# Performance work log

Hardware: AMD Instinct MI355X
Metric: run time of the kernel (lower is better)

Reference implementation:

```python
import jax, jax.numpy as jnp
import numpy as np

NUM_HEADS = 8
WINDOW = 3
LOCAL_LEN = WINDOW * WINDOW
SR_RATIO = 8


def _normalize(v, eps=1e-12):
    n = jnp.linalg.norm(v, axis=-1, keepdims=True)
    return v / jnp.maximum(n, eps)


def _layernorm(v, g, b, eps=1e-5):
    m = v.mean(-1, keepdims=True)
    var = ((v - m) ** 2).mean(-1, keepdims=True)
    return (v - m) / jnp.sqrt(var + eps) * g + b


def _unfold3(x, H, W):
    # x: [B, C, H, W] -> [B, C, 9, H*W]  (kernel 3, pad 1, stride 1; torch nn.Unfold layout)
    B, C = x.shape[0], x.shape[1]
    xp = jnp.pad(x, ((0, 0), (0, 0), (1, 1), (1, 1)))
    patches = jnp.stack([xp[:, :, di:di + H, dj:dj + W]
                         for di in range(WINDOW) for dj in range(WINDOW)], axis=2)
    return patches.reshape(B, C, LOCAL_LEN, H * W)


def _forward(x, relative_coords_table, seq_length_scale, q_w, q_b, kv_w, kv_b,
             temperature, query_embedding, sr_w, sr_b, norm_g, norm_b,
             cpb_fc1_w, cpb_fc1_b, cpb_fc2_w, cpb_fc2_b,
             rel_bias_local, learnable_tokens, learnable_bias,
             proj_w, proj_b, relative_pos_index, padding_mask, H, W):
    B, N, C = x.shape
    hd = C // NUM_HEADS
    pool_H, pool_W = H // SR_RATIO, W // SR_RATIO
    pool_len = pool_H * pool_W

    # ---- queries ----
    q = (x @ q_w.T + q_b).reshape(B, N, NUM_HEADS, hd).transpose(0, 2, 1, 3)  # [B,h,N,d]
    q_norm = _normalize(q)
    q_scaled = (q_norm + query_embedding) * jax.nn.softplus(temperature) * seq_length_scale

    # ---- local k/v via unfold ----
    kv = x @ kv_w.T + kv_b  # [B,N,2C]
    k_loc = _normalize(kv[..., :C].reshape(B, N, NUM_HEADS, hd)).reshape(B, N, C)
    kv_img = jnp.concatenate([k_loc, kv[..., C:]], -1).transpose(0, 2, 1).reshape(B, 2 * C, H, W)
    kv_unf = _unfold3(kv_img, H, W).reshape(B, 2 * NUM_HEADS, hd, LOCAL_LEN, N)
    kv_unf = kv_unf.transpose(0, 1, 4, 2, 3)  # [B,2h,N,d,9]
    k_local, v_local = kv_unf[:, :NUM_HEADS], kv_unf[:, NUM_HEADS:]

    attn_local = jnp.einsum('bhnd,bhndl->bhnl', q_scaled, k_local) + rel_bias_local[:, None, :]
    attn_local = jnp.where(padding_mask, -jnp.inf, attn_local)

    # ---- pooled global k/v ----
    x_img = x.transpose(0, 2, 1).reshape(B, C, H, W)
    x_sr = jax.nn.gelu(jnp.einsum('oc,bchw->bohw', sr_w, x_img) + sr_b[None, :, None, None],
                       approximate=False)
    x_pool = x_sr.reshape(B, C, pool_H, SR_RATIO, pool_W, SR_RATIO).mean((3, 5))
    x_pool = x_pool.reshape(B, C, pool_len).transpose(0, 2, 1)
    x_pool = _layernorm(x_pool, norm_g, norm_b)
    kv_p = (x_pool @ kv_w.T + kv_b).reshape(B, pool_len, 2 * NUM_HEADS, hd).transpose(0, 2, 1, 3)
    k_pool, v_pool = kv_p[:, :NUM_HEADS], kv_p[:, NUM_HEADS:]

    # ---- continuous relative position bias (extrapolation path) ----
    cpb = jax.nn.relu(relative_coords_table @ cpb_fc1_w.T + cpb_fc1_b) @ cpb_fc2_w.T + cpb_fc2_b  # [T,h]
    pool_bias = cpb[relative_pos_index].reshape(N, pool_len, NUM_HEADS).transpose(2, 0, 1)  # [h,N,P]

    attn_pool = jnp.einsum('bhnd,bhpd->bhnp', q_scaled, _normalize(k_pool)) + pool_bias

    attn = jax.nn.softmax(jnp.concatenate([attn_local, attn_pool], -1), axis=-1)
    a_loc, a_pool = attn[..., :LOCAL_LEN], attn[..., LOCAL_LEN:]

    lt = jnp.einsum('bhnd,hdl->bhnl', q_norm, learnable_tokens) + learnable_bias + a_loc
    x_local = jnp.einsum('bhnl,bhndl->bhnd', lt, v_local)
    x_p = jnp.einsum('bhnp,bhpd->bhnd', a_pool, v_pool)
    out = (x_local + x_p).transpose(0, 2, 1, 3).reshape(B, N, C)
    return out @ proj_w.T + proj_b


def setup_inputs() -> dict:
    key = jax.random.key(0)
    B, H, W, C = 4, 64, 64, 256
    N = H * W
    hd = C // NUM_HEADS
    pool_H, pool_W = H // SR_RATIO, W // SR_RATIO
    pool_len = pool_H * pool_W

    # padding mask + per-query valid window length (get_seqlen_and_mask)
    ii, jj = np.meshgrid(np.arange(H), np.arange(W), indexing='ij')
    cols = []
    for di in range(WINDOW):
        for dj in range(WINDOW):
            ni, nj = ii + di - 1, jj + dj - 1
            cols.append(((ni < 0) | (ni >= H) | (nj < 0) | (nj >= W)).reshape(-1))
    padding_mask = np.stack(cols, -1)  # [N, 9], True = outside image
    local_len = (~padding_mask).sum(-1, keepdims=True).astype(np.float32)
    seq_length_scale = np.log(local_len + pool_len)  # [N, 1]

    # get_relative_position_cpb((H,W), (pool_H,pool_W))
    axis_q = np.arange(H, dtype=np.float64)
    axis_k = axis_q.reshape(pool_H, SR_RATIO).mean(-1)
    kh, kw = np.meshgrid(axis_k, axis_k, indexing='ij')
    qh, qw = np.meshgrid(axis_q, axis_q, indexing='ij')
    rel_h = (qh.ravel()[:, None] - kh.ravel()[None, :]) / (H - 1) * 8
    rel_w = (qw.ravel()[:, None] - kw.ravel()[None, :]) / (W - 1) * 8
    rel = np.stack([rel_h, rel_w], -1).reshape(-1, 2)
    table, idx = np.unique(rel, axis=0, return_inverse=True)
    table = np.sign(table) * np.log2(np.abs(table) + 1.0) / np.log2(8.0)

    ks = jax.random.split(key, 12)

    def nrm(k, shape, std=0.02):
        return jax.random.normal(k, shape, jnp.float32) * std

    return {
        'x': jax.random.normal(ks[0], (B, N, C), jnp.float32),
        'relative_coords_table': jnp.asarray(table, jnp.float32),
        'seq_length_scale': jnp.asarray(seq_length_scale, jnp.float32),
        'q_w': nrm(ks[1], (C, C)), 'q_b': jnp.zeros((C,), jnp.float32),
        'kv_w': nrm(ks[2], (2 * C, C)), 'kv_b': jnp.zeros((2 * C,), jnp.float32),
        'temperature': jnp.full((NUM_HEADS, 1, 1), float(np.log(np.expm1(1.0 / 0.24))), jnp.float32),
        'query_embedding': nrm(ks[3], (NUM_HEADS, 1, hd)),
        'sr_w': nrm(ks[4], (C, C)), 'sr_b': jnp.zeros((C,), jnp.float32),
        'norm_g': jnp.ones((C,), jnp.float32), 'norm_b': jnp.zeros((C,), jnp.float32),
        'cpb_fc1_w': nrm(ks[5], (512, 2), 0.1), 'cpb_fc1_b': jnp.zeros((512,), jnp.float32),
        'cpb_fc2_w': nrm(ks[6], (NUM_HEADS, 512)), 'cpb_fc2_b': jnp.zeros((NUM_HEADS,), jnp.float32),
        'rel_bias_local': nrm(ks[7], (NUM_HEADS, LOCAL_LEN), 0.0004),
        'learnable_tokens': nrm(ks[8], (NUM_HEADS, hd, LOCAL_LEN)),
        'learnable_bias': jnp.zeros((NUM_HEADS, 1, LOCAL_LEN), jnp.float32),
        'proj_w': nrm(ks[9], (C, C)), 'proj_b': jnp.zeros((C,), jnp.float32),
        'relative_pos_index': jnp.asarray(idx, jnp.int32),
        'padding_mask': jnp.asarray(padding_mask),
        'H': H, 'W': W,
    }


def reference(x, relative_coords_table, seq_length_scale, q_w, q_b, kv_w, kv_b,
              temperature, query_embedding, sr_w, sr_b, norm_g, norm_b,
              cpb_fc1_w, cpb_fc1_b, cpb_fc2_w, cpb_fc2_b,
              rel_bias_local, learnable_tokens, learnable_bias,
              proj_w, proj_b, relative_pos_index, padding_mask, H, W):
    return _forward(x, relative_coords_table, seq_length_scale, q_w, q_b, kv_w, kv_b,
                    temperature, query_embedding, sr_w, sr_b, norm_g, norm_b,
                    cpb_fc1_w, cpb_fc1_b, cpb_fc2_w, cpb_fc2_b,
                    rel_bias_local, learnable_tokens, learnable_bias,
                    proj_w, proj_b, relative_pos_index, padding_mask, H, W)
```

## Files before the change

### kernel.cpp

```cpp
#include <hip/hip_runtime.h>
#include <math.h>


typedef unsigned short ushort_t;
typedef __attribute__((ext_vector_type(8))) _Float16 half8;
typedef __attribute__((ext_vector_type(2))) _Float16 half2_t;
typedef __attribute__((ext_vector_type(4))) float f32x4;
typedef __attribute__((ext_vector_type(4))) int int4_t;

static __device__ __forceinline__ ushort_t f2h(float f) {
    _Float16 h = (_Float16)f;
    return *(ushort_t*)&h;
}

static __device__ __forceinline__ float fdot2f(half2_t a, half2_t b, float c) {
#if __has_builtin(__builtin_amdgcn_fdot2)
    return __builtin_amdgcn_fdot2(a, b, c, false);
#else
    return (float)a[0] * (float)b[0] + (float)a[1] * (float)b[1] + c;
#endif
}

template <int CTRL>
static __device__ __forceinline__ float dpp_addf(float x) {
    int v = __builtin_amdgcn_update_dpp(
        0, __builtin_bit_cast(int, x), CTRL, 0xF, 0xF, true);
    return x + __builtin_bit_cast(float, v);
}
template <int CTRL>
static __device__ __forceinline__ float dpp_maxf(float x) {
    int v = __builtin_amdgcn_update_dpp(
        0, __builtin_bit_cast(int, x), CTRL, 0xF, 0xF, true);
    return fmaxf(x, __builtin_bit_cast(float, v));
}
static __device__ __forceinline__ float quad_sumf(float x) {
    return dpp_addf<0x4E>(dpp_addf<0xB1>(x));
}
static __device__ __forceinline__ float sum16f(float x) {
    return dpp_addf<0x128>(dpp_addf<0x124>(quad_sumf(x)));
}
static __device__ __forceinline__ float max16f(float x) {
    return dpp_maxf<0x128>(dpp_maxf<0x124>(dpp_maxf<0x4E>(dpp_maxf<0xB1>(x))));
}

#define GLOAD16(g, l)                                                        \
    __builtin_amdgcn_global_load_lds(                                        \
        (const __attribute__((address_space(1))) unsigned int*)(g),          \
        (__attribute__((address_space(3))) unsigned int*)(l), 16, 0, 0)

template <int TM, int TN, bool AHM>
__global__ __launch_bounds__(256) void mfma_hgemm(
    const ushort_t* __restrict__ Ag, const ushort_t* __restrict__ Bg,
    const float* __restrict__ bias, float* __restrict__ out0,
    ushort_t* __restrict__ qh_out, ushort_t* __restrict__ kvh,
    ushort_t* __restrict__ xsrh, int mode, int Arows)
{
    const int K = 256;
    const int IM = TM / 32;
    const int JN = TN / 32;
    constexpr int LPS = TM / 64 + TN / 64;
    __shared__ ushort_t Ah[2][TM * 32];
    __shared__ ushort_t Bh[2][TN * 32];

    const int t = threadIdx.x;
    const int w = t >> 6;
    const int lane = t & 63;

    const int nwg = gridDim.x * gridDim.y;
    int wg = blockIdx.y * gridDim.x + blockIdx.x;
    wg = (wg & 7) * (nwg >> 3) + (wg >> 3);
    const int bm = (wg / gridDim.x) * TM;
    const int bn = (wg % gridDim.x) * TN;

    const int wm = (w >> 1) * (TM / 2);
    const int wn = (w & 1) * (TN / 2);

    f32x4 acc[IM][JN];
#pragma unroll
    for (int i = 0; i < IM; ++i)
#pragma unroll
        for (int j = 0; j < JN; ++j) acc[i][j] = f32x4{0.f, 0.f, 0.f, 0.f};

    const int lrow  = t >> 2;
    const int lk8sw = ((t & 3) ^ ((t >> 3) & 3)) * 8;

#define STAGE(bufi, k0s)                                                     \
    do {                                                                     \
        _Pragma("unroll")                                                    \
        for (int r = 0; r < TM / 64; ++r) {                                  \
            const ushort_t* srcA = AHM                                       \
                ? Ag + ((size_t)((k0s) >> 5) * Arows + (bm + r * 64 + lrow)) * 32 + lk8sw \
                : Ag + (size_t)(bm + r * 64 + lrow) * K + (k0s) + lk8sw;     \
            GLOAD16(srcA, &Ah[bufi][(unsigned)(r * 64 + w * 16) * 32]);      \
        }                                                                    \
        _Pragma("unroll")                                                    \
        for (int r = 0; r < TN / 64; ++r)                                    \
            GLOAD16(Bg + (size_t)(bn + r * 64 + lrow) * K + (k0s) + lk8sw,   \
                    &Bh[bufi][(unsigned)(r * 64 + w * 16) * 32]);            \
    } while (0)

    const int fr   = lane & 15;
    const int sws8 = ((lane >> 4) ^ ((fr >> 1) & 3)) * 8;

#define COMPUTE(bufi)                                                        \
    do {                                                                     \
        half8 af[IM], bf[JN];                                                \
        _Pragma("unroll")                                                    \
        for (int i2 = 0; i2 < IM; ++i2)                                      \
            af[i2] = *(const half8*)&Ah[bufi][(unsigned)(wm + i2 * 16 + fr) * 32 + sws8]; \
        _Pragma("unroll")                                                    \
        for (int j2 = 0; j2 < JN; ++j2)                                      \
            bf[j2] = *(const half8*)&Bh[bufi][(unsigned)(wn + j2 * 16 + fr) * 32 + sws8]; \
        __builtin_amdgcn_s_setprio(1);                                       \
        _Pragma("unroll")                                                    \
        for (int i2 = 0; i2 < IM; ++i2)                                      \
            _Pragma("unroll")                                                \
            for (int j2 = 0; j2 < JN; ++j2)                                  \
                acc[i2][j2] = __builtin_amdgcn_mfma_f32_16x16x32_f16(        \
                    af[i2], bf[j2], acc[i2][j2], 0, 0, 0);                   \
        __builtin_amdgcn_s_setprio(0);                                       \
    } while (0)

    STAGE(0, 0);
    STAGE(1, 32);
    int buf = 0;
#pragma unroll
    for (int s = 0; s < K / 32 - 1; ++s) {
        asm volatile("s_waitcnt vmcnt(%0)" :: "n"(LPS) : "memory");
        __builtin_amdgcn_s_barrier();
        asm volatile("" ::: "memory");
        COMPUTE(buf);
        asm volatile("" ::: "memory");
        __builtin_amdgcn_s_barrier();
        asm volatile("" ::: "memory");
        if (s + 2 < K / 32) STAGE(buf, (s + 2) * 32);
        buf ^= 1;
    }
    asm volatile("s_waitcnt vmcnt(0)" ::: "memory");
    __builtin_amdgcn_s_barrier();
    asm volatile("" ::: "memory");
    COMPUTE(buf);
#undef COMPUTE
#undef STAGE

    const int q4 = (lane >> 4) * 4;
#pragma unroll
    for (int i = 0; i < IM; ++i) {
#pragma unroll
        for (int jp = 0; jp < JN / 2; ++jp) {
#pragma unroll
            for (int r = 0; r < 4; ++r) {
                const int row = bm + wm + i * 16 + q4 + r;
                const int col0 = bn + wn + jp * 32 + fr;
                const int col1 = col0 + 16;
                float v0 = acc[i][2 * jp][r] + bias[col0];
                float v1 = acc[i][2 * jp + 1][r] + bias[col1];
                if (mode == 0) {
                    if (col0 < 256) {
                        const size_t base = ((size_t)(col0 >> 5) * Arows + row) * 32;
                        qh_out[base + fr]      = f2h(v0);
                        qh_out[base + fr + 16] = f2h(v1);
                    } else if (col0 < 512) {
                        const float ss = sum16f(v0 * v0 + v1 * v1);
                        const float invn = 1.0f / fmaxf(sqrtf(ss), 1e-12f);
                        const size_t base = ((size_t)((col0 - 256) >> 5) * Arows + row) * 64;
                        kvh[base + fr]      = f2h(v0 * invn);
                        kvh[base + fr + 16] = f2h(v1 * invn);
                    } else if (col0 < 768) {
                        const size_t base = ((size_t)((col0 - 512) >> 5) * Arows + row) * 64 + 32;
                        kvh[base + fr]      = f2h(v0);
                        kvh[base + fr + 16] = f2h(v1);
                    } else {
                        v0 = 0.5f * v0 * (1.0f + erff(v0 * 0.70710678118654752f));
                        v1 = 0.5f * v1 * (1.0f + erff(v1 * 0.70710678118654752f));
                        xsrh[(size_t)row * 256 + (col0 - 768)] = f2h(v0);
                        xsrh[(size_t)row * 256 + (col1 - 768)] = f2h(v1);
                    }
                } else if (mode == 2) {
                    if (col0 < 256) {
                        const float ss = sum16f(v0 * v0 + v1 * v1);
                        const float invn = 1.0f / fmaxf(sqrtf(ss), 1e-12f);
                        const size_t base = ((size_t)(col0 >> 5) * Arows + row) * 64;
                        kvh[base + fr]      = f2h(v0 * invn);
                        kvh[base + fr + 16] = f2h(v1 * invn);
                    } else {
                        const size_t base = ((size_t)((col0 - 256) >> 5) * Arows + row) * 64 + 32;
                        kvh[base + fr]      = f2h(v0);
                        kvh[base + fr + 16] = f2h(v1);
                    }
                } else {
                    out0[(size_t)row * 256 + col0] = v0;
                    out0[(size_t)row * 256 + col1] = v1;
                }
            }
        }
    }
}

__global__ __launch_bounds__(256) void prep_cpb(
    const float4* __restrict__ x, ushort4* __restrict__ xh, int n4, int nprep,
    const float* __restrict__ qw, const float* __restrict__ kvw,
    const float* __restrict__ srw, const float* __restrict__ pw,
    const float* __restrict__ qb, const float* __restrict__ kvb,
    const float* __restrict__ srb,
    const int* __restrict__ rpi, ushort_t* __restrict__ rpi16,
    ushort_t* __restrict__ Wall, ushort_t* __restrict__ Pw,
    float* __restrict__ ball,
    const float* __restrict__ table, const float* __restrict__ w1,
    const float* __restrict__ b1, const float* __restrict__ w2,
    const float* __restrict__ b2, ushort_t* __restrict__ cpbT, int T)
{
    if (blockIdx.x >= nprep) {
        const int wv = threadIdx.x >> 6;
        const int lane = threadIdx.x & 63;
        const int row = (blockIdx.x - nprep) * 4 + wv;
        if (row >= T) return;
        const float t0 = table[(size_t)row * 2];
        const float t1 = table[(size_t)row * 2 + 1];
        const int base = lane * 8;

        const float4* w1p = (const float4*)(w1 + (size_t)base * 2);
        float4 wa = w1p[0], wb = w1p[1], wc = w1p[2], wd = w1p[3];
        float4 ba = *(const float4*)(b1 + base);
        float4 bb = *(const float4*)(b1 + base + 4);
        float h[8];
        h[0] = fmaxf(fmaf(t1, wa.y, fmaf(t0, wa.x, ba.x)), 0.f);
        h[1] = fmaxf(fmaf(t1, wa.w, fmaf(t0, wa.z, ba.y)), 0.f);
        h[2] = fmaxf(fmaf(t1, wb.y, fmaf(t0, wb.x, ba.z)), 0.f);
        h[3] = fmaxf(fmaf(t1, wb.w, fmaf(t0, wb.z, ba.w)), 0.f);
        h[4] = fmaxf(fmaf(t1, wc.y, fmaf(t0, wc.x, bb.x)), 0.f);
        h[5] = fmaxf(fmaf(t1, wc.w, fmaf(t0, wc.z, bb.y)), 0.f);
        h[6] = fmaxf(fmaf(t1, wd.y, fmaf(t0, wd.x, bb.z)), 0.f);
        h[7] = fmaxf(fmaf(t1, wd.w, fmaf(t0, wd.z, bb.w)), 0.f);

#pragma unroll
        for (int hh = 0; hh < 8; ++hh) {
            const float4* w2p = (const float4*)(w2 + (size_t)hh * 512 + base);
            float4 p0 = w2p[0], p1 = w2p[1];
            float s = h[0]*p0.x + h[1]*p0.y + h[2]*p0.z + h[3]*p0.w
                    + h[4]*p1.x + h[5]*p1.y + h[6]*p1.z + h[7]*p1.w;
#pragma unroll
            for (int off = 1; off <= 32; off <<= 1) s += __shfl_xor(s, off);
            if (lane == 0) cpbT[(size_t)hh * T + row] = f2h(s + b2[hh]);
        }
        return;
    }

    int idx = blockIdx.x * 256 + threadIdx.x;
    if (idx < n4) {
        float4 v = x[idx];
        ushort4 h;
        h.x = f2h(v.x); h.y = f2h(v.y); h.z = f2h(v.z); h.w = f2h(v.w);
        xh[idx] = h;
    }
    if (idx < 262144) {
        int nn = idx >> 8, k = idx & 255;
        float a;
        if (nn < 256)      a = qw[nn * 256 + k];
        else if (nn < 768) a = kvw[(nn - 256) * 256 + k];
        else               a = srw[(nn - 768) * 256 + k];
        Wall[idx] = f2h(a);
        rpi16[idx] = (ushort_t)rpi[idx];
    }
    if (idx < 65536) Pw[idx] = f2h(pw[idx]);
    if (idx < 1024) {
        float bv;
        if (idx < 256)      bv = qb[idx];
        else if (idx < 768) bv = kvb[idx - 256];
        else                bv = srb[idx - 768];
        ball[idx] = bv;
    }
}

__global__ __launch_bounds__(256) void pool_ln(
    const ushort_t* __restrict__ xsr, const float* __restrict__ g,
    const float* __restrict__ be, ushort_t* __restrict__ xpool, int Hh, int Ww)
{
    const int C = 256;
    const int Nn = Hh * Ww;
    int b = blockIdx.x >> 6;
    int pidx = blockIdx.x & 63;
    int ph = pidx >> 3, pw = pidx & 7;
    int tid = threadIdx.x;
    float s = 0.f;
    for (int si = 0; si < 8; ++si) {
        int i = ph * 8 + si;
        const ushort_t* rowp = xsr + ((size_t)b * Nn + (size_t)i * Ww + pw * 8) * C + tid;
#pragma unroll
        for (int sj = 0; sj < 8; ++sj)
            s += (float)(*(const _Float16*)&rowp[(size_t)sj * C]);
    }
    s *= (1.f / 64.f);
    __shared__ float red[256];
    red[tid] = s; __syncthreads();
    for (int st = 128; st; st >>= 1) { if (tid < st) red[tid] += red[tid + st]; __syncthreads(); }
    float mean = red[0] * (1.f / 256.f);
    __syncthreads();
    float dv = s - mean;
    red[tid] = dv * dv; __syncthreads();
    for (int st = 128; st; st >>= 1) { if (tid < st) red[tid] += red[tid + st]; __syncthreads(); }
    float var = red[0] * (1.f / 256.f);
    xpool[(size_t)blockIdx.x * C + tid] = f2h(dv * rsqrtf(var + 1e-5f) * g[tid] + be[tid]);
}

__global__ __launch_bounds__(256) void attn_v11(
    const ushort_t* __restrict__ qh_g,
    const ushort_t* __restrict__ kvh,
    const ushort_t* __restrict__ kvph,
    const ushort_t* __restrict__ rpi16,
    const ushort_t* __restrict__ cpbT,
    const float* __restrict__ sls, const float* __restrict__ temp,
    const float* __restrict__ qe, const float* __restrict__ rbl,
    const float* __restrict__ ltok, const float* __restrict__ lbias,
    ushort_t* __restrict__ attno,
    int Mtot, int T)
{
    const int h = blockIdx.y, b = blockIdx.z;
    const int t = threadIdx.x;
    const int i = blockIdx.x;
    const int w = t >> 6;
    const int lane = t & 63;

    __shared__ ushort_t kvloc[3 * 64 * 64];
    __shared__ ushort_t kvp[64 * 64];
    __shared__ ushort_t pb_s[64][66];
    __shared__ ushort_t Ps[64][72];
    __shared__ float mzp[64][2];
    __shared__ float lts[9][32];
    __shared__ float rbl_s[9], lb_s[9], qe_s[32];

    {
        const int lt8 = lane >> 3, ls = lane & 7;
#pragma unroll
        for (int it = 0; it < 6; ++it) {
            const int u = it * 4 + w;
            const int dr = u >> 3, kB = u & 7;
            const int srcRow = min(max(i - 1 + dr, 0), 63);
            const int tok = kB * 8 + lt8;
            GLOAD16(kvh + ((size_t)h * Mtot + b * 4096 + srcRow * 64) * 64
                        + (size_t)(tok * 8 + (ls ^ (tok & 7))) * 8,
                    &kvloc[(size_t)(dr * 64 + kB * 8) * 64]);
        }
#pragma unroll
        for (int it = 0; it < 2; ++it) {
            const int u = it * 4 + w;
            const int tok = u * 8 + lt8;
            GLOAD16(kvph + ((size_t)h * 256 + b * 64) * 64
                         + (size_t)(tok * 8 + (ls ^ (tok & 7))) * 8,
                    &kvp[(size_t)(u * 8) * 64]);
        }
    }
    {
        const ushort_t* rp16 = rpi16 + (size_t)i * 4096;
        const ushort_t* ctab = cpbT + (size_t)h * T;
        for (int u = t; u < 4096; u += 256)
            pb_s[u >> 6][u & 63] = ctab[rp16[u]];
        for (int u = t; u < 288; u += 256) lts[u % 9][u / 9] = ltok[h * 288 + u];
        if (t < 9)  { rbl_s[t] = rbl[h * 9 + t]; lb_s[t] = lbias[h * 9 + t]; }
        if (t >= 64 && t < 96) qe_s[t - 64] = qe[h * 32 + (t - 64)];
    }
    __syncthreads();

    const int qi = lane >> 2;
    const int g4 = lane & 3;
    const int co = g4 * 8;
    const int j = w * 16 + qi;
    const int n = i * 64 + j;
    const size_t gq = (size_t)b * 4096 + n;

    const float tm = temp[h];
    const float sp = (tm > 20.f) ? tm : log1pf(expf(tm));

    float qv[8];
    {
        const half8 q8 = *(const half8*)(qh_g + ((size_t)h * Mtot + gq) * 32 + co);
        float ss = 0.f;
#pragma unroll
        for (int d = 0; d < 8; ++d) { qv[d] = (float)q8[d]; ss += qv[d] * qv[d]; }
        ss = quad_sumf(ss);
        const float invn = 1.0f / fmaxf(sqrtf(ss), 1e-12f);
#pragma unroll
        for (int d = 0; d < 8; ++d) qv[d] *= invn;
    }

    float lt[9];
#pragma unroll
    for (int l = 0; l < 9; ++l) {
        float dl = 0.f;
        const float4* lw = (const float4*)&lts[l][co];
#pragma unroll
        for (int c4 = 0; c4 < 2; ++c4) {
            float4 w4 = lw[c4];
            dl += qv[4*c4+0]*w4.x + qv[4*c4+1]*w4.y + qv[4*c4+2]*w4.z + qv[4*c4+3]*w4.w;
        }
        dl = quad_sumf(dl);
        lt[l] = dl + lb_s[l];
    }

    const float scal = sp * sls[n];
    half2_t qhp[4];
#pragma unroll
    for (int c = 0; c < 4; ++c) {
        float a = (qv[2*c+0] + qe_s[co + 2*c+0]) * scal;
        float bq = (qv[2*c+1] + qe_s[co + 2*c+1]) * scal;
        qhp[c] = half2_t{(_Float16)a, (_Float16)bq};
    }

    float sl[9];
#pragma unroll
    for (int l = 0; l < 9; ++l) {
        const int di = l / 3 - 1, dj = l % 3 - 1;
        const int ii = i + di;
        const int jn = j + dj;
        const bool ok = (ii >= 0) && (ii < 64) && (jn >= 0) && (jn < 64);
        const int dr = di + 1;
        const int tokc = max(min(jn, 63), 0);
        const half8 k8 = *(const half8*)
            &kvloc[(size_t)((dr * 64 + tokc) * 8 + (g4 ^ (tokc & 7))) * 8];
        float dk = 0.f;
        dk = fdot2f(qhp[0], __builtin_shufflevector(k8, k8, 0, 1), dk);
        dk = fdot2f(qhp[1], __builtin_shufflevector(k8, k8, 2, 3), dk);
        dk = fdot2f(qhp[2], __builtin_shufflevector(k8, k8, 4, 5), dk);
        dk = fdot2f(qhp[3], __builtin_shufflevector(k8, k8, 6, 7), dk);
        dk = quad_sumf(dk);
        sl[l] = ok ? (dk + rbl_s[l]) : -INFINITY;
    }
    float m_l = sl[0];
#pragma unroll
    for (int l = 1; l < 9; ++l) m_l = fmaxf(m_l, sl[l]);

    const int fr = lane & 15;
    const int cn = lane >> 4;
    const int q4 = cn * 4;
    half8 af;
    {
        const int sidx = (4 * fr + cn) << 2;
        int4_t ai;
        ai.x = __builtin_amdgcn_ds_bpermute(sidx, __builtin_bit_cast(int, qhp[0]));
        ai.y = __builtin_amdgcn_ds_bpermute(sidx, __builtin_bit_cast(int, qhp[1]));
        ai.z = __builtin_amdgcn_ds_bpermute(sidx, __builtin_bit_cast(int, qhp[2]));
        ai.w = __builtin_amdgcn_ds_bpermute(sidx, __builtin_bit_cast(int, qhp[3]));
        af = __builtin_bit_cast(half8, ai);
    }
    f32x4 acc[4];
#pragma unroll
    for (int ct = 0; ct < 4; ++ct) {
#pragma unroll
        for (int r = 0; r < 4; ++r)
            acc[ct][r] = (float)(*(const _Float16*)&pb_s[w * 16 + q4 + r][ct * 16 + fr]);
    }
#pragma unroll
    for (int ct = 0; ct < 4; ++ct) {
        const int tok = ct * 16 + fr;
        const half8 bf = *(const half8*)&kvp[(size_t)(tok * 8 + (cn ^ (tok & 7))) * 8];
        acc[ct] = __builtin_amdgcn_mfma_f32_16x16x32_f16(af, bf, acc[ct], 0, 0, 0);
    }

#pragma unroll
    for (int r = 0; r < 4; ++r) {
        float mm = fmaxf(fmaxf(acc[0][r], acc[1][r]), fmaxf(acc[2][r], acc[3][r]));
        mm = max16f(mm);
        float z = 0.f;
        float pv[4];
#pragma unroll
        for (int ct = 0; ct < 4; ++ct) {
            pv[ct] = __expf(acc[ct][r] - mm);
            z += pv[ct];
        }
        z = sum16f(z);
#pragma unroll
        for (int ct = 0; ct < 4; ++ct)
            Ps[w * 16 + q4 + r][ct * 16 + fr] = f2h(pv[ct]);
        if (fr == 0) { mzp[w * 16 + q4 + r][0] = mm; mzp[w * 16 + q4 + r][1] = z; }
    }

    const float m_p = mzp[j][0];
    const float Z_p = mzp[j][1];
    const float m = fmaxf(m_l, m_p);
    const float fp = __expf(m_p - m);
    float Z = Z_p * fp;
    const _Float16 fh = (_Float16)fp;

    half2_t oh[4];
#pragma unroll
    for (int c = 0; c < 4; ++c) oh[c] = half2_t{(_Float16)0.f, (_Float16)0.f};

#pragma unroll
    for (int cch = 0; cch < 8; ++cch) {
        const half8 p8 = *(const half8*)&Ps[j][cch * 8];
#pragma unroll
        for (int k = 0; k < 8; ++k) {
            const int p = cch * 8 + k;
            const _Float16 ah = p8[k] * fh;
            const half2_t a2 = half2_t{ah, ah};
            const half8 v8 = *(const half8*)
                &kvp[(size_t)(p * 8 + ((4 + g4) ^ (p & 7))) * 8];
            oh[0] = a2 * __builtin_shufflevector(v8, v8, 0, 1) + oh[0];
            oh[1] = a2 * __builtin_shufflevector(v8, v8, 2, 3) + oh[1];
            oh[2] = a2 * __builtin_shufflevector(v8, v8, 4, 5) + oh[2];
            oh[3] = a2 * __builtin_shufflevector(v8, v8, 6, 7) + oh[3];
        }
    }

#pragma unroll
    for (int l = 0; l < 9; ++l) { sl[l] = __expf(sl[l] - m); Z += sl[l]; }

#pragma unroll
    for (int l = 0; l < 9; ++l) {
        const int di = l / 3 - 1, dj = l % 3 - 1;
        const int ii = i + di;
        const int jn = j + dj;
        const bool ok = (ii >= 0) && (ii < 64) && (jn >= 0) && (jn < 64);
        const int dr = di + 1;
        const int tokc = max(min(jn, 63), 0);
        const float coef = ok ? (sl[l] + lt[l] * Z) : 0.f;
        const half8 v8 = *(const half8*)
            &kvloc[(size_t)((dr * 64 + tokc) * 8 + ((4 + g4) ^ (tokc & 7))) * 8];
        const _Float16 ch = (_Float16)coef;
        const half2_t c2 = half2_t{ch, ch};
        oh[0] = c2 * __builtin_shufflevector(v8, v8, 0, 1) + oh[0];
        oh[1] = c2 * __builtin_shufflevector(v8, v8, 2, 3) + oh[1];
        oh[2] = c2 * __builtin_shufflevector(v8, v8, 4, 5) + oh[2];
        oh[3] = c2 * __builtin_shufflevector(v8, v8, 6, 7) + oh[3];
    }

    const float invZ = 1.0f / Z;
    ushort4* outp = (ushort4*)(attno + ((size_t)h * Mtot + gq) * 32 + co);
#pragma unroll
    for (int c4 = 0; c4 < 2; ++c4) {
        ushort4 u;
        u.x = f2h((float)oh[2*c4+0][0] * invZ);
        u.y = f2h((float)oh[2*c4+0][1] * invZ);
        u.z = f2h((float)oh[2*c4+1][0] * invZ);
        u.w = f2h((float)oh[2*c4+1][1] * invZ);
        outp[c4] = u;
    }
}

extern "C" void kernel_launch(void* const* d_in, const int* in_sizes, int n_in,
                              void* d_out, int out_size, void* d_ws, size_t ws_size,
                              hipStream_t stream)
{
    const float* x    = (const float*)d_in[0];
    const float* tbl  = (const float*)d_in[1];
    const float* sls  = (const float*)d_in[2];
    const float* q_w  = (const float*)d_in[3];
    const float* q_b  = (const float*)d_in[4];
    const float* kv_w = (const float*)d_in[5];
    const float* kv_b = (const float*)d_in[6];
    const float* temp = (const float*)d_in[7];
    const float* qe   = (const float*)d_in[8];
    const float* sr_w = (const float*)d_in[9];
    const float* sr_b = (const float*)d_in[10];
    const float* ng   = (const float*)d_in[11];
    const float* nb   = (const float*)d_in[12];
    const float* f1w  = (const float*)d_in[13];
    const float* f1b  = (const float*)d_in[14];
    const float* f2w  = (const float*)d_in[15];
    const float* f2b  = (const float*)d_in[16];
    const float* rbl  = (const float*)d_in[17];
    const float* ltok = (const float*)d_in[18];
    const float* lbias= (const float*)d_in[19];
    const float* pw   = (const float*)d_in[20];
    const float* pb   = (const float*)d_in[21];
    const int*   rpi  = (const int*)d_in[22];

    const int C = 256, Hh = 64, Ww = 64, Nn = Hh * Ww;
    const int B = in_sizes[0] / (Nn * C);
    const int T = in_sizes[1] / 2;
    const int M = B * Nn;

    float* ws = (float*)d_ws;
    size_t o = 0;
    ushort_t* qh    = (ushort_t*)(ws + o); o += (size_t)M * C / 2;
    ushort_t* kvh   = (ushort_t*)(ws + o); o += (size_t)M * C;
    ushort_t* xsrh  = (ushort_t*)(ws + o); o += (size_t)M * C / 2;
    ushort_t* xpoolh= (ushort_t*)(ws + o); o += (size_t)B * 64 * C / 2;
    ushort_t* kvph  = (ushort_t*)(ws + o); o += (size_t)B * 64 * C;
    ushort_t* cpbT  = (ushort_t*)(ws + o); o += (size_t)T * 4 + 4;
    ushort_t* rpi16 = (ushort_t*)(ws + o); o += 131072;
    ushort_t* xh   = (ushort_t*)(ws + o); o += (size_t)M * C / 2;
    ushort_t* Wall = (ushort_t*)(ws + o); o += 1024 * 256 / 2;
    ushort_t* Pwh  = (ushort_t*)(ws + o); o += 256 * 256 / 2;
    float* ball = ws + o; o += 1024;
    ushort_t* attno_hf = xh;

    dim3 blk(256);
    const int n4x = M * C / 4;
    const int nprep = (n4x + 255) / 256;
    const int ncpb  = (T + 3) / 4;

    prep_cpb<<<nprep + ncpb, blk, 0, stream>>>(
        (const float4*)x, (ushort4*)xh, n4x,
        nprep, q_w, kv_w, sr_w, pw, q_b, kv_b, sr_b, rpi, rpi16,
        Wall, Pwh, ball, tbl, f1w, f1b, f2w, f2b, cpbT, T);
    mfma_hgemm<128, 128, false><<<dim3(8, M / 128), blk, 0, stream>>>(
        xh, Wall, ball, nullptr, qh, kvh, xsrh, 0, M);
    pool_ln<<<B * 64, blk, 0, stream>>>(xsrh, ng, nb, xpoolh, Hh, Ww);
    mfma_hgemm<64, 64, false><<<dim3(8, (B * 64) / 64), blk, 0, stream>>>(
        xpoolh, Wall + 256 * 256, ball + 256, nullptr, nullptr, kvph, nullptr, 2, B * 64);
    attn_v11<<<dim3(64, 8, B), blk, 0, stream>>>(
        qh, kvh, kvph, rpi16, cpbT, sls, temp, qe, rbl, ltok, lbias, attno_hf, M, T);
    mfma_hgemm<128, 128, true><<<dim3(2, M / 128), blk, 0, stream>>>(
        attno_hf, Pwh, pb, (float*)d_out, nullptr, nullptr, nullptr, 1, M);
}
```

Before: 228.9 us.

## Read local K/V from global, merge LDS buffers, vectorise prep, retune GEMM tiles

```diff
diff --git a/kernel.cpp b/kernel.cpp
--- a/kernel.cpp
+++ b/kernel.cpp
@@ -253,16 +253,29 @@
         h.x = f2h(v.x); h.y = f2h(v.y); h.z = f2h(v.z); h.w = f2h(v.w);
         xh[idx] = h;
     }
-    if (idx < 262144) {
-        int nn = idx >> 8, k = idx & 255;
-        float a;
-        if (nn < 256)      a = qw[nn * 256 + k];
-        else if (nn < 768) a = kvw[(nn - 256) * 256 + k];
-        else               a = srw[(nn - 768) * 256 + k];
-        Wall[idx] = f2h(a);
-        rpi16[idx] = (ushort_t)rpi[idx];
-    }
-    if (idx < 65536) Pw[idx] = f2h(pw[idx]);
+    if (idx < 65536) {
+        const int base = idx * 4;
+        const int nn = base >> 8, k = base & 255;
+        const float* src;
+        if (nn < 256)      src = qw + (size_t)nn * 256 + k;
+        else if (nn < 768) src = kvw + (size_t)(nn - 256) * 256 + k;
+        else               src = srw + (size_t)(nn - 768) * 256 + k;
+        const float4 a = *(const float4*)src;
+        ushort4 hw;
+        hw.x = f2h(a.x); hw.y = f2h(a.y); hw.z = f2h(a.z); hw.w = f2h(a.w);
+        *(ushort4*)&Wall[base] = hw;
+        const int4 rv = *(const int4*)&rpi[base];
+        ushort4 r4;
+        r4.x = (ushort_t)rv.x; r4.y = (ushort_t)rv.y;
+        r4.z = (ushort_t)rv.z; r4.w = (ushort_t)rv.w;
+        *(ushort4*)&rpi16[base] = r4;
+    }
+    if (idx < 16384) {
+        const float4 a = *(const float4*)&pw[(size_t)idx * 4];
+        ushort4 hw;
+        hw.x = f2h(a.x); hw.y = f2h(a.y); hw.z = f2h(a.z); hw.w = f2h(a.w);
+        *(ushort4*)&Pw[(size_t)idx * 4] = hw;
+    }
     if (idx < 1024) {
         float bv;
         if (idx < 256)      bv = qb[idx];
@@ -303,7 +316,7 @@
     xpool[(size_t)blockIdx.x * C + tid] = f2h(dv * rsqrtf(var + 1e-5f) * g[tid] + be[tid]);
 }
 
-__global__ __launch_bounds__(256) void attn_v11(
+__global__ __launch_bounds__(256) void attn_v12(
     const ushort_t* __restrict__ qh_g,
     const ushort_t* __restrict__ kvh,
     const ushort_t* __restrict__ kvph,
@@ -321,26 +334,14 @@
     const int w = t >> 6;
     const int lane = t & 63;
 
-    __shared__ ushort_t kvloc[3 * 64 * 64];
     __shared__ ushort_t kvp[64 * 64];
-    __shared__ ushort_t pb_s[64][66];
-    __shared__ ushort_t Ps[64][72];
+    __shared__ ushort_t pbPs[64][72];
     __shared__ float mzp[64][2];
     __shared__ float lts[9][32];
     __shared__ float rbl_s[9], lb_s[9], qe_s[32];
 
     {
         const int lt8 = lane >> 3, ls = lane & 7;
-#pragma unroll
-        for (int it = 0; it < 6; ++it) {
-            const int u = it * 4 + w;
-            const int dr = u >> 3, kB = u & 7;
-            const int srcRow = min(max(i - 1 + dr, 0), 63);
-            const int tok = kB * 8 + lt8;
-            GLOAD16(kvh + ((size_t)h * Mtot + b * 4096 + srcRow * 64) * 64
-                        + (size_t)(tok * 8 + (ls ^ (tok & 7))) * 8,
-                    &kvloc[(size_t)(dr * 64 + kB * 8) * 64]);
-        }
 #pragma unroll
         for (int it = 0; it < 2; ++it) {
             const int u = it * 4 + w;
@@ -354,7 +355,7 @@
         const ushort_t* rp16 = rpi16 + (size_t)i * 4096;
         const ushort_t* ctab = cpbT + (size_t)h * T;
         for (int u = t; u < 4096; u += 256)
-            pb_s[u >> 6][u & 63] = ctab[rp16[u]];
+            pbPs[u >> 6][u & 63] = ctab[rp16[u]];
         for (int u = t; u < 288; u += 256) lts[u % 9][u / 9] = ltok[h * 288 + u];
         if (t < 9)  { rbl_s[t] = rbl[h * 9 + t]; lb_s[t] = lbias[h * 9 + t]; }
         if (t >= 64 && t < 96) qe_s[t - 64] = qe[h * 32 + (t - 64)];
@@ -367,6 +368,7 @@
     const int j = w * 16 + qi;
     const int n = i * 64 + j;
     const size_t gq = (size_t)b * 4096 + n;
+    const ushort_t* kvb = kvh + ((size_t)h * Mtot + (size_t)b * 4096) * 64;
 
     const float tm = temp[h];
     const float sp = (tm > 20.f) ? tm : log1pf(expf(tm));
@@ -413,10 +415,9 @@
         const int ii = i + di;
         const int jn = j + dj;
         const bool ok = (ii >= 0) && (ii < 64) && (jn >= 0) && (jn < 64);
-        const int dr = di + 1;
-        const int tokc = max(min(jn, 63), 0);
-        const half8 k8 = *(const half8*)
-            &kvloc[(size_t)((dr * 64 + tokc) * 8 + (g4 ^ (tokc & 7))) * 8];
+        const int ic = max(min(ii, 63), 0);
+        const int jc = max(min(jn, 63), 0);
+        const half8 k8 = *(const half8*)&kvb[(size_t)(ic * 64 + jc) * 64 + co];
         float dk = 0.f;
         dk = fdot2f(qhp[0], __builtin_shufflevector(k8, k8, 0, 1), dk);
         dk = fdot2f(qhp[1], __builtin_shufflevector(k8, k8, 2, 3), dk);
@@ -447,7 +448,7 @@
     for (int ct = 0; ct < 4; ++ct) {
 #pragma unroll
         for (int r = 0; r < 4; ++r)
-            acc[ct][r] = (float)(*(const _Float16*)&pb_s[w * 16 + q4 + r][ct * 16 + fr]);
+            acc[ct][r] = (float)(*(const _Float16*)&pbPs[w * 16 + q4 + r][ct * 16 + fr]);
     }
 #pragma unroll
     for (int ct = 0; ct < 4; ++ct) {
@@ -470,7 +471,7 @@
         z = sum16f(z);
 #pragma unroll
         for (int ct = 0; ct < 4; ++ct)
-            Ps[w * 16 + q4 + r][ct * 16 + fr] = f2h(pv[ct]);
+            pbPs[w * 16 + q4 + r][ct * 16 + fr] = f2h(pv[ct]);
         if (fr == 0) { mzp[w * 16 + q4 + r][0] = mm; mzp[w * 16 + q4 + r][1] = z; }
     }
 
@@ -487,7 +488,7 @@
 
 #pragma unroll
     for (int cch = 0; cch < 8; ++cch) {
-        const half8 p8 = *(const half8*)&Ps[j][cch * 8];
+        const half8 p8 = *(const half8*)&pbPs[j][cch * 8];
 #pragma unroll
         for (int k = 0; k < 8; ++k) {
             const int p = cch * 8 + k;
@@ -511,11 +512,10 @@
         const int ii = i + di;
         const int jn = j + dj;
         const bool ok = (ii >= 0) && (ii < 64) && (jn >= 0) && (jn < 64);
-        const int dr = di + 1;
-        const int tokc = max(min(jn, 63), 0);
+        const int ic = max(min(ii, 63), 0);
+        const int jc = max(min(jn, 63), 0);
         const float coef = ok ? (sl[l] + lt[l] * Z) : 0.f;
-        const half8 v8 = *(const half8*)
-            &kvloc[(size_t)((dr * 64 + tokc) * 8 + ((4 + g4) ^ (tokc & 7))) * 8];
+        const half8 v8 = *(const half8*)&kvb[(size_t)(ic * 64 + jc) * 64 + 32 + co];
         const _Float16 ch = (_Float16)coef;
         const half2_t c2 = half2_t{ch, ch};
         oh[0] = c2 * __builtin_shufflevector(v8, v8, 0, 1) + oh[0];
@@ -594,13 +594,13 @@
         (const float4*)x, (ushort4*)xh, n4x,
         nprep, q_w, kv_w, sr_w, pw, q_b, kv_b, sr_b, rpi, rpi16,
         Wall, Pwh, ball, tbl, f1w, f1b, f2w, f2b, cpbT, T);
-    mfma_hgemm<128, 128, false><<<dim3(8, M / 128), blk, 0, stream>>>(
+    mfma_hgemm<128, 64, false><<<dim3(16, M / 128), blk, 0, stream>>>(
         xh, Wall, ball, nullptr, qh, kvh, xsrh, 0, M);
     pool_ln<<<B * 64, blk, 0, stream>>>(xsrh, ng, nb, xpoolh, Hh, Ww);
     mfma_hgemm<64, 64, false><<<dim3(8, (B * 64) / 64), blk, 0, stream>>>(
         xpoolh, Wall + 256 * 256, ball + 256, nullptr, nullptr, kvph, nullptr, 2, B * 64);
-    attn_v11<<<dim3(64, 8, B), blk, 0, stream>>>(
+    attn_v12<<<dim3(64, 8, B), blk, 0, stream>>>(
         qh, kvh, kvph, rpi16, cpbT, sls, temp, qe, rbl, ltok, lbias, attno_hf, M, T);
-    mfma_hgemm<128, 128, true><<<dim3(2, M / 128), blk, 0, stream>>>(
+    mfma_hgemm<64, 64, true><<<dim3(4, M / 64), blk, 0, stream>>>(
         attno_hf, Pwh, pb, (float*)d_out, nullptr, nullptr, nullptr, 1, M);
 }
```

Result: faster. 208.0 us (-9.1%).
